# Optimization experiments

Hardware: AMD Instinct MI355X
Metric: run time of the kernel (lower is better)

The kernel has to match this reference:

```python
import jax, jax.numpy as jnp
import numpy as np

N_ITEMS = 100000
K_IL = 64

def setup_inputs() -> dict:
    key = jax.random.key(0)
    k1, k2, k3 = jax.random.split(key, 3)
    X = jax.random.randint(k1, (1024, 10, 4), 0, N_ITEMS, dtype=jnp.int64)
    IL = jax.random.normal(k2, (N_ITEMS, K_IL), dtype=jnp.float32)
    LI = jax.random.normal(k3, (N_ITEMS, K_IL), dtype=jnp.float32)
    return {"X": X, "IL": IL, "LI": LI, "tag": 0}

def reference(X, IL, LI, tag):
    # tag==0 path: score every item for each row's previous item.
    # predictions[b, i] = sum_k IL[i, k] * LI[prev[b], k] / sqrt(k_IL)
    prev = X[:, -2, 3]                       # [B] previous item ids
    li_prev = LI[prev]                       # [B, K] gather
    scale = 1.0 / (IL.shape[1] ** 0.5)
    return jnp.einsum('bk,ik->bi', li_prev, IL) * scale  # [B, N_ITEMS]
```

## Files before the change

### kernel.cpp

```cpp
#include <hip/hip_runtime.h>


typedef short short8 __attribute__((ext_vector_type(8)));
typedef float f32x4 __attribute__((ext_vector_type(4)));
typedef unsigned short ushort4v __attribute__((ext_vector_type(4)));
typedef unsigned short ushort8v __attribute__((ext_vector_type(8)));

#define KDIM  64
#define LDSS  72
#define MSLAB 256
#define NSLAB 256
#define NCH   32

static __device__ __forceinline__ unsigned short f2bf(float f) {
    unsigned u = __float_as_uint(f);
    return (unsigned short)((u + 0x7fffu + ((u >> 16) & 1u)) >> 16);
}

static __device__ __forceinline__ short8 cvt8(float4 v0, float4 v1) {
    union { ushort8v u; short8 s; } r;
    r.u[0] = f2bf(v0.x); r.u[1] = f2bf(v0.y); r.u[2] = f2bf(v0.z); r.u[3] = f2bf(v0.w);
    r.u[4] = f2bf(v1.x); r.u[5] = f2bf(v1.y); r.u[6] = f2bf(v1.z); r.u[7] = f2bf(v1.w);
    return r.s;
}

__global__ __launch_bounds__(256)
void fpmc_gather(const int* __restrict__ X, const float* __restrict__ LI,
                 unsigned short* __restrict__ ws, int M) {
    const int t = threadIdx.x;
    const int r = blockIdx.x * 16 + (t >> 4);
    if (r >= M) return;
    const int c = (t & 15) * 4;
    const int idx = X[r * 40 + 35];
    const float4 v = *(const float4*)(LI + (size_t)idx * KDIM + c);
    ushort4v p;
    p.x = f2bf(v.x); p.y = f2bf(v.y); p.z = f2bf(v.z); p.w = f2bf(v.w);
    *(ushort4v*)(ws + (size_t)r * KDIM + c) = p;
}

template<bool USE_WS>
__global__ __launch_bounds__(256, 4)
void fpmc_gemm2(const int* __restrict__ X, const float* __restrict__ IL,
                const float* __restrict__ LI, const unsigned short* __restrict__ Aws,
                float* __restrict__ out, int M, int N) {
    __shared__ __align__(16) unsigned short As[MSLAB * LDSS];

    const int t  = threadIdx.x;
    const int m0 = blockIdx.y * MSLAB;
    const int i0 = blockIdx.x * NSLAB;

    if (USE_WS) {
        #pragma unroll
        for (int it = 0; it < 8; ++it) {
            const int chunk = it * 256 + t;
            const int r = chunk >> 3;
            const int c = (chunk & 7) * 8;
            ushort8v v = *(const ushort8v*)(Aws + (size_t)(m0 + r) * KDIM + c);
            *(ushort8v*)&As[r * LDSS + c] = v;
        }
    } else {
        const int rb = t >> 4;
        const int c  = (t & 15) * 4;
        #pragma unroll
        for (int it = 0; it < MSLAB / 16; ++it) {
            const int r = it * 16 + rb;
            const int idx = X[(m0 + r) * 40 + 35];
            const float4 v = *(const float4*)(LI + (size_t)idx * KDIM + c);
            ushort4v p;
            p.x = f2bf(v.x); p.y = f2bf(v.y); p.z = f2bf(v.z); p.w = f2bf(v.w);
            *(ushort4v*)&As[r * LDSS + c] = p;
        }
    }
    __syncthreads();

    const int w    = t >> 6;
    const int l    = t & 63;
    const int lr   = l & 15;
    const int quad = l >> 4;
    const int mwav = w * 64;
    const float scale = 0.125f;

    for (int nc = 0; nc < NSLAB / NCH; ++nc) {
        const int n0c = i0 + nc * NCH;

        f32x4 acc[4][2];
        #pragma unroll
        for (int mt = 0; mt < 4; ++mt)
            #pragma unroll
            for (int nt = 0; nt < 2; ++nt)
                acc[mt][nt] = (f32x4){0.f, 0.f, 0.f, 0.f};

        #pragma unroll
        for (int ks = 0; ks < 2; ++ks) {
            short8 b[2];
            #pragma unroll
            for (int nt = 0; nt < 2; ++nt) {
                int n = n0c + nt * 16 + lr;
                if (n > N - 1) n = N - 1;
                const float* p = IL + (size_t)n * KDIM + ks * 32 + quad * 8;
                b[nt] = cvt8(*(const float4*)p, *(const float4*)(p + 4));
            }
            short8 a[4];
            #pragma unroll
            for (int mt = 0; mt < 4; ++mt)
                a[mt] = *(const short8*)&As[(mwav + mt * 16 + lr) * LDSS + ks * 32 + quad * 8];
            #pragma unroll
            for (int mt = 0; mt < 4; ++mt)
                #pragma unroll
                for (int nt = 0; nt < 2; ++nt)
                    acc[mt][nt] = __builtin_amdgcn_mfma_f32_16x16x32_bf16(
                        b[nt], a[mt], acc[mt][nt], 0, 0, 0);
        }

        #pragma unroll
        for (int mt = 0; mt < 4; ++mt) {
            const int m = m0 + mwav + mt * 16 + lr;
            if (m >= M) continue;
            float* orow = out + (size_t)m * N;
            #pragma unroll
            for (int nt = 0; nt < 2; ++nt) {
                const int n = n0c + nt * 16 + quad * 4;
                if (n < N) {
                    f32x4 v = acc[mt][nt] * scale;
                    __builtin_nontemporal_store(v, (f32x4*)(orow + n));
                }
            }
        }
    }
}

extern "C" void kernel_launch(void* const* d_in, const int* in_sizes, int n_in,
                              void* d_out, int out_size, void* d_ws, size_t ws_size,
                              hipStream_t stream) {
    const int*   X  = (const int*)d_in[0];
    const float* IL = (const float*)d_in[1];
    const float* LI = (const float*)d_in[2];
    float* out = (float*)d_out;

    const int M = in_sizes[0] / 40;
    const int N = in_sizes[1] / KDIM;

    unsigned short* Aws = (unsigned short*)d_ws;
    const size_t need = (size_t)M * KDIM * sizeof(unsigned short);

    dim3 grid((N + NSLAB - 1) / NSLAB, (M + MSLAB - 1) / MSLAB);
    if (d_ws != nullptr && ws_size >= need) {
        fpmc_gather<<<dim3((M + 15) / 16), dim3(256), 0, stream>>>(X, LI, Aws, M);
        fpmc_gemm2<true><<<grid, dim3(256), 0, stream>>>(X, IL, LI, Aws, out, M, N);
    } else {
        fpmc_gemm2<false><<<grid, dim3(256), 0, stream>>>(X, IL, LI, Aws, out, M, N);
    }
}
```

Before: 484.1 us.

## Pre-convert IL to bf16 and software-pipeline B loads in GEMM

Adds a kernel that converts the whole IL matrix to bf16 in workspace once per call, so the GEMM reads half the bytes for B and skips repeated per-block conversion. It also hoists the A fragments out of the N loop into registers and prefetches the next chunk's B fragments while the current chunk's MFMAs and stores run. The cost is an extra full pass over IL (read fp32, write bf16) and more register pressure. The M bound check on stores was also removed.

Result: slower. 504.3 us (+4.2%).

```diff
diff --git a/kernel.cpp b/kernel.cpp
--- a/kernel.cpp
+++ b/kernel.cpp
@@ -26,7 +26,7 @@
 
 __global__ __launch_bounds__(256)
 void fpmc_gather(const int* __restrict__ X, const float* __restrict__ LI,
-                 unsigned short* __restrict__ ws, int M) {
+                 unsigned short* __restrict__ Abf, int M) {
     const int t = threadIdx.x;
     const int r = blockIdx.x * 16 + (t >> 4);
     if (r >= M) return;
@@ -35,13 +35,29 @@
     const float4 v = *(const float4*)(LI + (size_t)idx * KDIM + c);
     ushort4v p;
     p.x = f2bf(v.x); p.y = f2bf(v.y); p.z = f2bf(v.z); p.w = f2bf(v.w);
-    *(ushort4v*)(ws + (size_t)r * KDIM + c) = p;
-}
-
-template<bool USE_WS>
+    *(ushort4v*)(Abf + (size_t)r * KDIM + c) = p;
+}
+
+__global__ __launch_bounds__(256)
+void fpmc_cvt(const float* __restrict__ IL, unsigned short* __restrict__ ILbf,
+              int total) {
+    const int tid = blockIdx.x * 256 + threadIdx.x;
+    const int base = tid * 16;
+    if (base >= total) return;
+    const float4* src = (const float4*)(IL + base);
+    ushort8v* dst = (ushort8v*)(ILbf + base);
+    union { ushort8v u; short8 s; } a, b;
+    a.s = cvt8(src[0], src[1]);
+    b.s = cvt8(src[2], src[3]);
+    dst[0] = a.u;
+    dst[1] = b.u;
+}
+
+template<int MODE>
 __global__ __launch_bounds__(256, 4)
-void fpmc_gemm2(const int* __restrict__ X, const float* __restrict__ IL,
-                const float* __restrict__ LI, const unsigned short* __restrict__ Aws,
+void fpmc_gemm3(const int* __restrict__ X, const float* __restrict__ IL,
+                const float* __restrict__ LI, const unsigned short* __restrict__ ILbf,
+                const unsigned short* __restrict__ Abf,
                 float* __restrict__ out, int M, int N) {
     __shared__ __align__(16) unsigned short As[MSLAB * LDSS];
 
@@ -49,13 +65,13 @@
     const int m0 = blockIdx.y * MSLAB;
     const int i0 = blockIdx.x * NSLAB;
 
-    if (USE_WS) {
+    if (MODE >= 1) {
         #pragma unroll
         for (int it = 0; it < 8; ++it) {
             const int chunk = it * 256 + t;
             const int r = chunk >> 3;
             const int c = (chunk & 7) * 8;
-            ushort8v v = *(const ushort8v*)(Aws + (size_t)(m0 + r) * KDIM + c);
+            ushort8v v = *(const ushort8v*)(Abf + (size_t)(m0 + r) * KDIM + c);
             *(ushort8v*)&As[r * LDSS + c] = v;
         }
     } else {
@@ -80,8 +96,40 @@
     const int mwav = w * 64;
     const float scale = 0.125f;
 
+    short8 a[2][4];
+    #pragma unroll
+    for (int ks = 0; ks < 2; ++ks)
+        #pragma unroll
+        for (int mt = 0; mt < 4; ++mt)
+            a[ks][mt] = *(const short8*)&As[(mwav + mt * 16 + lr) * LDSS + ks * 32 + quad * 8];
+
+    auto loadB = [&](int nc, short8 b[2][2]) {
+        const int n0c = i0 + nc * NCH;
+        #pragma unroll
+        for (int nt = 0; nt < 2; ++nt) {
+            int n = n0c + nt * 16 + lr;
+            if (n > N - 1) n = N - 1;
+            if (MODE == 2) {
+                const ushort8v* p = (const ushort8v*)(ILbf + (size_t)n * KDIM);
+                union { ushort8v u; short8 s; } r0, r1;
+                r0.u = p[quad];
+                r1.u = p[4 + quad];
+                b[0][nt] = r0.s;
+                b[1][nt] = r1.s;
+            } else {
+                const float* p = IL + (size_t)n * KDIM + quad * 8;
+                b[0][nt] = cvt8(*(const float4*)p, *(const float4*)(p + 4));
+                b[1][nt] = cvt8(*(const float4*)(p + 32), *(const float4*)(p + 36));
+            }
+        }
+    };
+
+    short8 bc[2][2], bn[2][2];
+    loadB(0, bc);
+
+    #pragma unroll 1
     for (int nc = 0; nc < NSLAB / NCH; ++nc) {
-        const int n0c = i0 + nc * NCH;
+        if (nc + 1 < NSLAB / NCH) loadB(nc + 1, bn);
 
         f32x4 acc[4][2];
         #pragma unroll
@@ -91,31 +139,18 @@
                 acc[mt][nt] = (f32x4){0.f, 0.f, 0.f, 0.f};
 
         #pragma unroll
-        for (int ks = 0; ks < 2; ++ks) {
-            short8 b[2];
-            #pragma unroll
-            for (int nt = 0; nt < 2; ++nt) {
-                int n = n0c + nt * 16 + lr;
-                if (n > N - 1) n = N - 1;
-                const float* p = IL + (size_t)n * KDIM + ks * 32 + quad * 8;
-                b[nt] = cvt8(*(const float4*)p, *(const float4*)(p + 4));
-            }
-            short8 a[4];
-            #pragma unroll
-            for (int mt = 0; mt < 4; ++mt)
-                a[mt] = *(const short8*)&As[(mwav + mt * 16 + lr) * LDSS + ks * 32 + quad * 8];
+        for (int ks = 0; ks < 2; ++ks)
             #pragma unroll
             for (int mt = 0; mt < 4; ++mt)
                 #pragma unroll
                 for (int nt = 0; nt < 2; ++nt)
                     acc[mt][nt] = __builtin_amdgcn_mfma_f32_16x16x32_bf16(
-                        b[nt], a[mt], acc[mt][nt], 0, 0, 0);
-        }
-
+                        bc[ks][nt], a[ks][mt], acc[mt][nt], 0, 0, 0);
+
+        const int n0c = i0 + nc * NCH;
         #pragma unroll
         for (int mt = 0; mt < 4; ++mt) {
             const int m = m0 + mwav + mt * 16 + lr;
-            if (m >= M) continue;
             float* orow = out + (size_t)m * N;
             #pragma unroll
             for (int nt = 0; nt < 2; ++nt) {
@@ -126,6 +161,12 @@
                 }
             }
         }
+
+        #pragma unroll
+        for (int ks = 0; ks < 2; ++ks)
+            #pragma unroll
+            for (int nt = 0; nt < 2; ++nt)
+                bc[ks][nt] = bn[ks][nt];
     }
 }
 
@@ -140,14 +181,24 @@
     const int M = in_sizes[0] / 40;
     const int N = in_sizes[1] / KDIM;
 
-    unsigned short* Aws = (unsigned short*)d_ws;
-    const size_t need = (size_t)M * KDIM * sizeof(unsigned short);
+    const size_t ilbf_bytes = (size_t)N * KDIM * sizeof(unsigned short);
+    const size_t a_bytes    = (size_t)M * KDIM * sizeof(unsigned short);
+
+    unsigned short* ILbf = (unsigned short*)d_ws;
+    unsigned short* Abf  = (unsigned short*)((char*)d_ws + ilbf_bytes);
 
     dim3 grid((N + NSLAB - 1) / NSLAB, (M + MSLAB - 1) / MSLAB);
-    if (d_ws != nullptr && ws_size >= need) {
-        fpmc_gather<<<dim3((M + 15) / 16), dim3(256), 0, stream>>>(X, LI, Aws, M);
-        fpmc_gemm2<true><<<grid, dim3(256), 0, stream>>>(X, IL, LI, Aws, out, M, N);
+
+    if (d_ws != nullptr && ws_size >= ilbf_bytes + a_bytes) {
+        const int total = N * KDIM;
+        fpmc_gather<<<dim3((M + 15) / 16), dim3(256), 0, stream>>>(X, LI, Abf, M);
+        fpmc_cvt<<<dim3((total / 16 + 255) / 256), dim3(256), 0, stream>>>(IL, ILbf, total);
+        fpmc_gemm3<2><<<grid, dim3(256), 0, stream>>>(X, IL, LI, ILbf, Abf, out, M, N);
+    } else if (d_ws != nullptr && ws_size >= a_bytes) {
+        unsigned short* A0 = (unsigned short*)d_ws;
+        fpmc_gather<<<dim3((M + 15) / 16), dim3(256), 0, stream>>>(X, LI, A0, M);
+        fpmc_gemm3<1><<<grid, dim3(256), 0, stream>>>(X, IL, LI, nullptr, A0, out, M, N);
     } else {
-        fpmc_gemm2<false><<<grid, dim3(256), 0, stream>>>(X, IL, LI, Aws, out, M, N);
+        fpmc_gemm3<0><<<grid, dim3(256), 0, stream>>>(X, IL, LI, nullptr, nullptr, out, M, N);
     }
 }
```

## Pre-convert IL to bf16 and restructure GEMM into thin 16-row strips with prefetch

Applied to the files above, without the earlier changes.

A combined prep kernel converts the whole IL matrix to bf16 in the workspace and also gathers the LI rows. The GEMM is restructured so each 512-thread block handles 16 output rows across a wide N range. A-fragments stay in registers, so LDS is no longer used, and B tiles are triple-buffered in registers so loads are issued two chunks ahead. This removes the repeated fp32 IL loads and conversions done by every M-slab. The cost is an extra full pass over IL, and IL is now re-read once per 16-row strip from cache. The output stores also switch from nontemporal to regular stores.

Result: slower. 495.2 us (+2.3%).

```diff
diff --git a/kernel.cpp b/kernel.cpp
--- a/kernel.cpp
+++ b/kernel.cpp
@@ -6,11 +6,12 @@
 typedef unsigned short ushort4v __attribute__((ext_vector_type(4)));
 typedef unsigned short ushort8v __attribute__((ext_vector_type(8)));
 
-#define KDIM  64
-#define LDSS  72
-#define MSLAB 256
-#define NSLAB 256
-#define NCH   32
+#define KDIM   64
+#define MROWS  16
+#define NWAVES 8
+#define NCHUNK 32
+#define JCH    49
+#define NBLK   (NWAVES * JCH * NCHUNK)
 
 static __device__ __forceinline__ unsigned short f2bf(float f) {
     unsigned u = __float_as_uint(f);
@@ -25,106 +26,115 @@
 }
 
 __global__ __launch_bounds__(256)
-void fpmc_gather(const int* __restrict__ X, const float* __restrict__ LI,
-                 unsigned short* __restrict__ ws, int M) {
+void fpmc_prep(const int* __restrict__ X, const float* __restrict__ IL,
+               const float* __restrict__ LI, unsigned short* __restrict__ ILbf,
+               unsigned short* __restrict__ Abf, int M, int total, int cvtBlocks) {
+    const int b = blockIdx.x;
     const int t = threadIdx.x;
-    const int r = blockIdx.x * 16 + (t >> 4);
-    if (r >= M) return;
-    const int c = (t & 15) * 4;
-    const int idx = X[r * 40 + 35];
-    const float4 v = *(const float4*)(LI + (size_t)idx * KDIM + c);
-    ushort4v p;
-    p.x = f2bf(v.x); p.y = f2bf(v.y); p.z = f2bf(v.z); p.w = f2bf(v.w);
-    *(ushort4v*)(ws + (size_t)r * KDIM + c) = p;
-}
-
-template<bool USE_WS>
-__global__ __launch_bounds__(256, 4)
-void fpmc_gemm2(const int* __restrict__ X, const float* __restrict__ IL,
-                const float* __restrict__ LI, const unsigned short* __restrict__ Aws,
-                float* __restrict__ out, int M, int N) {
-    __shared__ __align__(16) unsigned short As[MSLAB * LDSS];
-
-    const int t  = threadIdx.x;
-    const int m0 = blockIdx.y * MSLAB;
-    const int i0 = blockIdx.x * NSLAB;
-
-    if (USE_WS) {
-        #pragma unroll
-        for (int it = 0; it < 8; ++it) {
-            const int chunk = it * 256 + t;
-            const int r = chunk >> 3;
-            const int c = (chunk & 7) * 8;
-            ushort8v v = *(const ushort8v*)(Aws + (size_t)(m0 + r) * KDIM + c);
-            *(ushort8v*)&As[r * LDSS + c] = v;
+    if (b < cvtBlocks) {
+        const int base = (b * 256 + t) * 16;
+        if (base < total) {
+            const float4* src = (const float4*)(IL + base);
+            ushort8v* dst = (ushort8v*)(ILbf + base);
+            union { ushort8v u; short8 s; } a0, a1;
+            a0.s = cvt8(src[0], src[1]);
+            a1.s = cvt8(src[2], src[3]);
+            dst[0] = a0.u;
+            dst[1] = a1.u;
         }
     } else {
-        const int rb = t >> 4;
-        const int c  = (t & 15) * 4;
-        #pragma unroll
-        for (int it = 0; it < MSLAB / 16; ++it) {
-            const int r = it * 16 + rb;
-            const int idx = X[(m0 + r) * 40 + 35];
+        const int r = (b - cvtBlocks) * 16 + (t >> 4);
+        if (r < M) {
+            const int c = (t & 15) * 4;
+            const int idx = X[r * 40 + 35];
             const float4 v = *(const float4*)(LI + (size_t)idx * KDIM + c);
             ushort4v p;
             p.x = f2bf(v.x); p.y = f2bf(v.y); p.z = f2bf(v.z); p.w = f2bf(v.w);
-            *(ushort4v*)&As[r * LDSS + c] = p;
+            *(ushort4v*)(Abf + (size_t)r * KDIM + c) = p;
         }
     }
-    __syncthreads();
+}
 
+template<int MODE>
+__global__ __launch_bounds__(512, 4)
+void fpmc_gemm4(const int* __restrict__ X, const float* __restrict__ IL,
+                const float* __restrict__ LI, const unsigned short* __restrict__ ILbf,
+                const unsigned short* __restrict__ Abf,
+                float* __restrict__ out, int M, int N) {
+    const int b  = blockIdx.x;
+    const int bx = b & 7;
+    const int by = b >> 3;
+    const int t    = threadIdx.x;
     const int w    = t >> 6;
     const int l    = t & 63;
     const int lr   = l & 15;
     const int quad = l >> 4;
-    const int mwav = w * 64;
+    const int m0 = by * MROWS;
+    const int i0 = bx * NBLK;
     const float scale = 0.125f;
 
-    for (int nc = 0; nc < NSLAB / NCH; ++nc) {
-        const int n0c = i0 + nc * NCH;
+    short8 a[2];
+    if (MODE == 1) {
+        const ushort8v* pa = (const ushort8v*)(Abf + (size_t)(m0 + lr) * KDIM);
+        union { ushort8v u; short8 s; } r0, r1;
+        r0.u = pa[quad];
+        r1.u = pa[4 + quad];
+        a[0] = r0.s;
+        a[1] = r1.s;
+    } else {
+        const int idx = X[(m0 + lr) * 40 + 35];
+        const float* p = LI + (size_t)idx * KDIM + quad * 8;
+        a[0] = cvt8(*(const float4*)p,        *(const float4*)(p + 4));
+        a[1] = cvt8(*(const float4*)(p + 32), *(const float4*)(p + 36));
+    }
 
-        f32x4 acc[4][2];
+    auto loadB = [&](int j, short8 bq[2][2]) {
+        const int n0c = i0 + (j * NWAVES + w) * NCHUNK;
         #pragma unroll
-        for (int mt = 0; mt < 4; ++mt)
+        for (int nt = 0; nt < 2; ++nt) {
+            int n = n0c + nt * 16 + lr;
+            if (n > N - 1) n = N - 1;
+            if (MODE == 1) {
+                const ushort8v* p = (const ushort8v*)(ILbf + (size_t)n * KDIM);
+                union { ushort8v u; short8 s; } r0, r1;
+                r0.u = p[quad];
+                r1.u = p[4 + quad];
+                bq[0][nt] = r0.s;
+                bq[1][nt] = r1.s;
+            } else {
+                const float* p = IL + (size_t)n * KDIM + quad * 8;
+                bq[0][nt] = cvt8(*(const float4*)p,        *(const float4*)(p + 4));
+                bq[1][nt] = cvt8(*(const float4*)(p + 32), *(const float4*)(p + 36));
+            }
+        }
+    };
+
+    short8 bq[3][2][2];
+    loadB(0, bq[0]);
+    loadB(1, bq[1]);
+
+    #pragma unroll
+    for (int j = 0; j < JCH; ++j) {
+        if (j + 2 < JCH) loadB(j + 2, bq[(j + 2) % 3]);
+
+        f32x4 acc[2];
+        acc[0] = (f32x4){0.f, 0.f, 0.f, 0.f};
+        acc[1] = (f32x4){0.f, 0.f, 0.f, 0.f};
+
+        #pragma unroll
+        for (int ks = 0; ks < 2; ++ks)
             #pragma unroll
             for (int nt = 0; nt < 2; ++nt)
-                acc[mt][nt] = (f32x4){0.f, 0.f, 0.f, 0.f};
+                acc[nt] = __builtin_amdgcn_mfma_f32_16x16x32_bf16(
+                    bq[j % 3][ks][nt], a[ks], acc[nt], 0, 0, 0);
 
+        const int n0c = i0 + (j * NWAVES + w) * NCHUNK;
+        float* orow = out + (size_t)(m0 + lr) * N;
         #pragma unroll
-        for (int ks = 0; ks < 2; ++ks) {
-            short8 b[2];
-            #pragma unroll
-            for (int nt = 0; nt < 2; ++nt) {
-                int n = n0c + nt * 16 + lr;
-                if (n > N - 1) n = N - 1;
-                const float* p = IL + (size_t)n * KDIM + ks * 32 + quad * 8;
-                b[nt] = cvt8(*(const float4*)p, *(const float4*)(p + 4));
-            }
-            short8 a[4];
-            #pragma unroll
-            for (int mt = 0; mt < 4; ++mt)
-                a[mt] = *(const short8*)&As[(mwav + mt * 16 + lr) * LDSS + ks * 32 + quad * 8];
-            #pragma unroll
-            for (int mt = 0; mt < 4; ++mt)
-                #pragma unroll
-                for (int nt = 0; nt < 2; ++nt)
-                    acc[mt][nt] = __builtin_amdgcn_mfma_f32_16x16x32_bf16(
-                        b[nt], a[mt], acc[mt][nt], 0, 0, 0);
-        }
-
-        #pragma unroll
-        for (int mt = 0; mt < 4; ++mt) {
-            const int m = m0 + mwav + mt * 16 + lr;
-            if (m >= M) continue;
-            float* orow = out + (size_t)m * N;
-            #pragma unroll
-            for (int nt = 0; nt < 2; ++nt) {
-                const int n = n0c + nt * 16 + quad * 4;
-                if (n < N) {
-                    f32x4 v = acc[mt][nt] * scale;
-                    __builtin_nontemporal_store(v, (f32x4*)(orow + n));
-                }
-            }
+        for (int nt = 0; nt < 2; ++nt) {
+            const int n = n0c + nt * 16 + quad * 4;
+            if (n < N)
+                *(f32x4*)(orow + n) = acc[nt] * scale;
         }
     }
 }
@@ -140,14 +150,23 @@
     const int M = in_sizes[0] / 40;
     const int N = in_sizes[1] / KDIM;
 
-    unsigned short* Aws = (unsigned short*)d_ws;
-    const size_t need = (size_t)M * KDIM * sizeof(unsigned short);
+    const size_t ilbf_bytes = (size_t)N * KDIM * sizeof(unsigned short);
+    const size_t a_bytes    = (size_t)M * KDIM * sizeof(unsigned short);
 
-    dim3 grid((N + NSLAB - 1) / NSLAB, (M + MSLAB - 1) / MSLAB);
-    if (d_ws != nullptr && ws_size >= need) {
-        fpmc_gather<<<dim3((M + 15) / 16), dim3(256), 0, stream>>>(X, LI, Aws, M);
-        fpmc_gemm2<true><<<grid, dim3(256), 0, stream>>>(X, IL, LI, Aws, out, M, N);
+    const int gx = (N + NBLK - 1) / NBLK;
+    const int gy = (M + MROWS - 1) / MROWS;
+    dim3 grid(gx * gy);
+
+    if (d_ws != nullptr && ws_size >= ilbf_bytes + a_bytes && gx == 8) {
+        unsigned short* ILbf = (unsigned short*)d_ws;
+        unsigned short* Abf  = (unsigned short*)((char*)d_ws + ilbf_bytes);
+        const int total = N * KDIM;
+        const int cvtBlocks = (total / 16 + 255) / 256;
+        const int gatherBlocks = (M + 15) / 16;
+        fpmc_prep<<<dim3(cvtBlocks + gatherBlocks), dim3(256), 0, stream>>>(
+            X, IL, LI, ILbf, Abf, M, total, cvtBlocks);
+        fpmc_gemm4<1><<<grid, dim3(512), 0, stream>>>(X, IL, LI, ILbf, Abf, out, M, N);
     } else {
-        fpmc_gemm2<false><<<grid, dim3(256), 0, stream>>>(X, IL, LI, Aws, out, M, N);
+        fpmc_gemm4<0><<<grid, dim3(512), 0, stream>>>(X, IL, LI, nullptr, nullptr, out, M, N);
     }
 }
```
